# Performance work log

Hardware: AMD Instinct MI355X
Metric: run time of the kernel (lower is better)

The kernel has to match this reference:

```python
import jax, jax.numpy as jnp
import numpy as np

N = 32768       # total nodes across the batch of graphs
E = 524288      # total edges
D = 512         # feature dim (dimensions = [512, 512, 512])
G = 512         # number of graphs (64 nodes each)


def setup_inputs() -> dict:
    key = jax.random.key(0)
    ks = jax.random.split(key, 16)
    inp = {
        'feat': jax.random.normal(ks[0], (N, D), jnp.float32),
        'src': jax.random.randint(ks[1], (E,), 0, N, jnp.int32),
        'dst': jax.random.randint(ks[2], (E,), 0, N, jnp.int32),
        'adj_vals': jax.random.uniform(ks[3], (E,), jnp.float32),
        'graph_ids': (jnp.arange(N, dtype=jnp.int32) // (N // G)),
        'W0': jax.random.normal(ks[4], (D, D), jnp.float32) * 0.05,
        'b0': jnp.zeros((D,), jnp.float32),
        'W1': jax.random.normal(ks[5], (D, D), jnp.float32) * 0.05,
        'b1': jnp.zeros((D,), jnp.float32),
        'gW1': jax.random.normal(ks[6], (D, D), jnp.float32) * 0.05,
        'gb1': jnp.zeros((D,), jnp.float32),
        'gW2': jax.random.normal(ks[7], (D, D), jnp.float32) * 0.05,
        'gb2': jnp.zeros((D,), jnp.float32),
        'gW3': jax.random.normal(ks[8], (D, D), jnp.float32) * 0.05,
        'gb3': jnp.zeros((D,), jnp.float32),
        'gWs': jax.random.normal(ks[9], (D, D), jnp.float32) * 0.05,
        'gbs': jnp.zeros((D,), jnp.float32),
    }
    return inp


def reference(feat, src, dst, adj_vals, graph_ids,
              W0, b0, W1, b1,
              gW1, gb1, gW2, gb2, gW3, gb3, gWs, gbs):
    # GCN layer: act(A_hat @ (X W) + b), A_hat given as weighted edge list
    def gcn(h, W, b, act):
        support = h @ W                              # [N, D]
        msg = adj_vals[:, None] * support[src]       # [E, D]
        agg = jax.ops.segment_sum(msg, dst, num_segments=N)
        return act(agg + b)

    h = gcn(feat, W0, b0, jax.nn.relu)               # hidden layer, act=relu
    h = gcn(h, W1, b1, lambda x: x)                  # last layer, identity act

    # pooling: per-graph mean readout -> sigmoid -> repeat-expand back to nodes
    ones = jnp.ones((N, 1), h.dtype)
    counts = jax.ops.segment_sum(ones, graph_ids, num_segments=G)   # [G, 1]
    pooled = jax.ops.segment_sum(h, graph_ids, num_segments=G) / counts
    g = jax.nn.sigmoid(pooled)[graph_ids]            # [N, D] repeat-expanded

    z = jax.nn.relu(g @ gW1 + gb1)
    z = jax.nn.relu(z @ gW2 + gb2)
    z = jax.nn.relu(z @ gW3 + gb3)
    return z + (g @ gWs + gbs)
```

## Files before the change

kernel.cpp:

```cpp
#include <hip/hip_runtime.h>

typedef unsigned int u32;
typedef unsigned short u16;

typedef __attribute__((ext_vector_type(8))) __bf16 bf16x8;
typedef __attribute__((ext_vector_type(4))) float f32x4;
typedef __attribute__((ext_vector_type(2))) float f32x2;
typedef __attribute__((ext_vector_type(4))) u32 u32x4;

#define N_NODES 32768
#define N_EDGES 524288
#define DIM 512
#define N_GRAPHS 512
#define ECAP_ROW 1536
#define ECAP 1216
#define ELDS_SZ (ECAP + ECAP / 32 + 1)
#define NB_CONV 8192
#define NB_TR 1536

__device__ __forceinline__ u16 f2b(float f) {
  union { float f; u32 u; } v; v.f = f;
  u32 r = v.u + 0x7FFFu + ((v.u >> 16) & 1u);
  return (u16)(r >> 16);
}
__device__ __forceinline__ u32 pack2(float a, float b) {
  return (u32)f2b(a) | ((u32)f2b(b) << 16);
}
__device__ __forceinline__ float blo(u32 u) { union { u32 u; float f; } v; v.u = u << 16; return v.f; }
__device__ __forceinline__ float bhi(u32 u) { union { u32 u; float f; } v; v.u = u & 0xFFFF0000u; return v.f; }
__device__ __forceinline__ float b2f(u16 u) { union { u32 u; float f; } v; v.u = ((u32)u) << 16; return v.f; }

__device__ __forceinline__ void async16(const void* g, void* l) {
  __builtin_amdgcn_global_load_lds(
      (const __attribute__((address_space(1))) u32*)g,
      (__attribute__((address_space(3))) u32*)l, 16, 0, 0);
}

__device__ __forceinline__ int eidx(int i) { return i + (i >> 5); }

__device__ __forceinline__ void acc8(f32x2* a, u32x4 raw, float v) {
  f32x2 v2 = {v, v};
  a[0] += v2 * f32x2{blo(raw.x), bhi(raw.x)};
  a[1] += v2 * f32x2{blo(raw.y), bhi(raw.y)};
  a[2] += v2 * f32x2{blo(raw.z), bhi(raw.z)};
  a[3] += v2 * f32x2{blo(raw.w), bhi(raw.w)};
}

struct WPack {
  const float* src[6];
  u16* dst[6];
};
__global__ __launch_bounds__(256)
void k_prep(const float* __restrict__ feat, u16* __restrict__ featb, WPack wp,
            const int* __restrict__ dstv, int* __restrict__ counts) {
  __shared__ float tile[32][33];
  const int bid = blockIdx.x, tid = threadIdx.x;
  if (bid < NB_CONV) {
    int i = bid * 256 + tid;
    const float4* p = (const float4*)feat;
    float4 a = p[2 * i], b = p[2 * i + 1];
    uint4 o;
    o.x = pack2(a.x, a.y); o.y = pack2(a.z, a.w);
    o.z = pack2(b.x, b.y); o.w = pack2(b.z, b.w);
    ((uint4*)featb)[i] = o;
  } else if (bid < NB_CONV + NB_TR) {
    int idx = bid - NB_CONV;
    int bz = idx >> 8, rem = idx & 255, by = rem >> 4, bx = rem & 15;
    const float* W = wp.src[bz];
    u16* Wt = wp.dst[bz];
    int tx = tid & 31, ty = tid >> 5;
    int bx32 = bx * 32, by32 = by * 32;
    #pragma unroll
    for (int i = 0; i < 4; i++)
      tile[ty + 8 * i][tx] = W[(size_t)(by32 + ty + 8 * i) * DIM + bx32 + tx];
    __syncthreads();
    #pragma unroll
    for (int i = 0; i < 4; i++)
      Wt[(size_t)(bx32 + ty + 8 * i) * DIM + by32 + tx] = f2b(tile[tx][ty + 8 * i]);
  } else {
    int i = (bid - NB_CONV - NB_TR) * 256 + tid;
    atomicAdd(&counts[dstv[i]], 1);
  }
}

__global__ void k_scan(const int* __restrict__ counts, int* __restrict__ offsets,
                       int* __restrict__ cursor) {
  __shared__ int part[1024];
  int t = threadIdx.x;
  const int4* c4 = (const int4*)counts;
  int4 cv[8];
  #pragma unroll
  for (int j = 0; j < 8; j++) cv[j] = c4[t * 8 + j];
  int loc[32];
  int s = 0;
  #pragma unroll
  for (int j = 0; j < 8; j++) {
    loc[4 * j + 0] = s; s += cv[j].x;
    loc[4 * j + 1] = s; s += cv[j].y;
    loc[4 * j + 2] = s; s += cv[j].z;
    loc[4 * j + 3] = s; s += cv[j].w;
  }
  part[t] = s;
  __syncthreads();
  for (int off = 1; off < 1024; off <<= 1) {
    int v = (t >= off) ? part[t - off] : 0;
    __syncthreads();
    part[t] += v;
    __syncthreads();
  }
  int excl = (t == 0) ? 0 : part[t - 1];
  #pragma unroll
  for (int j = 0; j < 8; j++) {
    int4 o = make_int4(excl + loc[4 * j], excl + loc[4 * j + 1],
                       excl + loc[4 * j + 2], excl + loc[4 * j + 3]);
    ((int4*)offsets)[t * 8 + j] = o;
    ((int4*)cursor)[t * 8 + j] = o;
  }
  if (t == 1023) offsets[N_NODES] = excl + s;
}

__global__ void k_fill(const int* __restrict__ src, const int* __restrict__ dst,
                       const float* __restrict__ vals, int* __restrict__ cursor,
                       int2* __restrict__ epack) {
  int i = blockIdx.x * 256 + threadIdx.x;
  if (i >= N_EDGES) return;
  int d = dst[i];
  int p = atomicAdd(&cursor[d], 1);
  epack[p] = make_int2(src[i] | ((d & 63) << 15), __float_as_int(vals[i]));
}

__global__ __launch_bounds__(256)
void k_gemm_bt(const u16* __restrict__ A, const u16* __restrict__ Bt,
               u16* __restrict__ Cout, int M, int Nout, int K) {
  __shared__ __align__(16) u16 As[128 * 32];
  __shared__ __align__(16) u16 Bs[128 * 32];
  const int tid = threadIdx.x;
  const int l = tid & 63;
  const int w = tid >> 6;
  const int mBase = blockIdx.x * 128;
  const int nBase = blockIdx.y * 128;
  const int wm = (w >> 1) * 64;
  const int wn = (w & 1) * 64;
  const int lrow = l >> 2;
  const int lcol = (l & 3) * 8;
  const int q = l >> 4;
  const int r = l & 15;
  f32x4 acc[4][4] = {};

  for (int k0 = 0; k0 < K; k0 += 32) {
    #pragma unroll
    for (int p = 0; p < 2; p++) {
      int row = w * 32 + p * 16 + lrow;
      async16(A + (size_t)(mBase + row) * K + k0 + lcol, (char*)As + w * 2048 + p * 1024);
      async16(Bt + (size_t)(nBase + row) * K + k0 + lcol, (char*)Bs + w * 2048 + p * 1024);
    }
    __syncthreads();
    bf16x8 af[4], bfr[4];
    #pragma unroll
    for (int i = 0; i < 4; i++) af[i] = *(const bf16x8*)&As[(wm + i * 16 + r) * 32 + q * 8];
    #pragma unroll
    for (int j = 0; j < 4; j++) bfr[j] = *(const bf16x8*)&Bs[(wn + j * 16 + r) * 32 + q * 8];
    #pragma unroll
    for (int i = 0; i < 4; i++)
      #pragma unroll
      for (int j = 0; j < 4; j++)
        acc[i][j] = __builtin_amdgcn_mfma_f32_16x16x32_bf16(af[i], bfr[j], acc[i][j], 0, 0, 0);
    __syncthreads();
  }

  #pragma unroll
  for (int i = 0; i < 4; i++) {
    #pragma unroll
    for (int j = 0; j < 4; j++) {
      int col = nBase + wn + j * 16 + r;
      #pragma unroll
      for (int reg = 0; reg < 4; reg++) {
        int rowg = mBase + wm + i * 16 + q * 4 + reg;
        Cout[(size_t)rowg * Nout + col] = f2b(acc[i][j][reg]);
      }
    }
  }
}

template <bool RELU, bool ADDEND, bool OUTF32, bool SIGMOID>
__global__ __launch_bounds__(256)
void k_gemm_small(const u16* __restrict__ A, const u16* __restrict__ Bt,
                  const float* __restrict__ bias, const u16* __restrict__ addend,
                  void* __restrict__ Cout, int Nout, int K) {
  __shared__ __align__(16) u16 As[64 * 32];
  __shared__ __align__(16) u16 Bs[64 * 32];
  const int tid = threadIdx.x;
  const int l = tid & 63;
  const int w = tid >> 6;
  const int mBase = blockIdx.x * 64;
  const int nBase = blockIdx.y * 64;
  const int wm = (w >> 1) * 32;
  const int wn = (w & 1) * 32;
  const int lrow = tid >> 2;
  const int lcol = (tid & 3) * 8;
  const int q = l >> 4;
  const int r = l & 15;
  f32x4 acc[2][2] = {};

  for (int k0 = 0; k0 < K; k0 += 32) {
    async16(A + (size_t)(mBase + lrow) * K + k0 + lcol, (char*)As + tid * 16);
    async16(Bt + (size_t)(nBase + lrow) * K + k0 + lcol, (char*)Bs + tid * 16);
    __syncthreads();
    bf16x8 af[2], bfr[2];
    #pragma unroll
    for (int i = 0; i < 2; i++) af[i] = *(const bf16x8*)&As[(wm + i * 16 + r) * 32 + q * 8];
    #pragma unroll
    for (int j = 0; j < 2; j++) bfr[j] = *(const bf16x8*)&Bs[(wn + j * 16 + r) * 32 + q * 8];
    #pragma unroll
    for (int i = 0; i < 2; i++)
      #pragma unroll
      for (int j = 0; j < 2; j++)
        acc[i][j] = __builtin_amdgcn_mfma_f32_16x16x32_bf16(af[i], bfr[j], acc[i][j], 0, 0, 0);
    __syncthreads();
  }

  #pragma unroll
  for (int i = 0; i < 2; i++) {
    #pragma unroll
    for (int j = 0; j < 2; j++) {
      int col = nBase + wn + j * 16 + r;
      float bv = bias[col];
      #pragma unroll
      for (int reg = 0; reg < 4; reg++) {
        int rowg = mBase + wm + i * 16 + q * 4 + reg;
        float v = acc[i][j][reg] + bv;
        if (ADDEND) v += b2f(addend[(size_t)rowg * Nout + col]);
        if (RELU) v = fmaxf(v, 0.0f);
        if (SIGMOID) v = 1.0f / (1.0f + expf(-v));
        if (OUTF32) ((float*)Cout)[(size_t)rowg * Nout + col] = v;
        else ((u16*)Cout)[(size_t)rowg * Nout + col] = f2b(v);
      }
    }
  }
}

__global__ __launch_bounds__(256)
void k_agg_row(const u16* __restrict__ support, const int* __restrict__ offsets,
               const int2* __restrict__ epack, const float* __restrict__ bias,
               u16* __restrict__ outp) {
  __shared__ int2 eLds[ECAP_ROW];
  const int chunk = blockIdx.x & 7;
  const int cidx  = blockIdx.x >> 3;
  const int rowBase = cidx * 64;
  const int e0b = offsets[rowBase];
  const int nb = offsets[rowBase + 64] - e0b;
  for (int i = threadIdx.x; i < min(nb, ECAP_ROW); i += 256)
    eLds[i] = epack[e0b + i];
  __syncthreads();

  const int wi = threadIdx.x >> 6;
  const int l  = threadIdx.x & 63;
  const int grp = l >> 3;
  const int li  = l & 7;
  const int colOff = chunk * 64 + li * 8;
  const u16* spc = support + colOff;

  f32x2 b[4];
  {
    const float4* bp = (const float4*)(bias + colOff);
    float4 x = bp[0], y = bp[1];
    b[0] = f32x2{x.x, x.y}; b[1] = f32x2{x.z, x.w};
    b[2] = f32x2{y.x, y.y}; b[3] = f32x2{y.z, y.w};
  }

  #pragma unroll
  for (int pass = 0; pass < 2; pass++) {
    int r = rowBase + wi * 16 + pass * 8 + grp;
    int re0 = offsets[r] - e0b;
    int deg = offsets[r + 1] - e0b - re0;

    f32x2 a[4] = {b[0], b[1], b[2], b[3]};

    if (nb <= ECAP_ROW) {
      int i = 0;
      for (; i + 4 <= deg; i += 4) {
        int2 p0 = eLds[re0 + i];
        int2 p1 = eLds[re0 + i + 1];
        int2 p2 = eLds[re0 + i + 2];
        int2 p3 = eLds[re0 + i + 3];
        u32x4 r0 = *(const u32x4*)(spc + (size_t)(p0.x & 32767) * DIM);
        u32x4 r1 = *(const u32x4*)(spc + (size_t)(p1.x & 32767) * DIM);
        u32x4 r2 = *(const u32x4*)(spc + (size_t)(p2.x & 32767) * DIM);
        u32x4 r3 = *(const u32x4*)(spc + (size_t)(p3.x & 32767) * DIM);
        acc8(a, r0, __int_as_float(p0.y));
        acc8(a, r1, __int_as_float(p1.y));
        acc8(a, r2, __int_as_float(p2.y));
        acc8(a, r3, __int_as_float(p3.y));
      }
      for (; i < deg; i++) {
        int2 p = eLds[re0 + i];
        u32x4 raw = *(const u32x4*)(spc + (size_t)(p.x & 32767) * DIM);
        acc8(a, raw, __int_as_float(p.y));
      }
    } else {
      for (int i = 0; i < deg; i++) {
        int gi = re0 + i;
        int2 p = (gi < ECAP_ROW) ? eLds[gi] : epack[e0b + gi];
        u32x4 raw = *(const u32x4*)(spc + (size_t)(p.x & 32767) * DIM);
        acc8(a, raw, __int_as_float(p.y));
      }
    }

    #pragma unroll
    for (int i = 0; i < 4; i++) {
      a[i].x = fmaxf(a[i].x, 0.0f);
      a[i].y = fmaxf(a[i].y, 0.0f);
    }
    u32x4 o;
    o.x = pack2(a[0].x, a[0].y); o.y = pack2(a[1].x, a[1].y);
    o.z = pack2(a[2].x, a[2].y); o.w = pack2(a[3].x, a[3].y);
    *(u32x4*)(outp + (size_t)r * DIM + colOff) = o;
  }
}

__global__ __launch_bounds__(256)
void k_agg_pool(const u16* __restrict__ support, const int* __restrict__ offsets,
                const int2* __restrict__ epack, u16* __restrict__ outp) {
  __shared__ int2 eLds[ELDS_SZ];
  __shared__ float redLds[256];

  const int tid = threadIdx.x;
  const int chunk = blockIdx.x & 7;
  const int cidx = blockIdx.x >> 3;
  const int rowBase = cidx * 64;
  const int e0b = offsets[rowBase];
  const int nb = offsets[rowBase + 64] - e0b;
  const bool fits = (nb <= ECAP);

  if (fits) {
    for (int i = tid; i < nb; i += 256) eLds[eidx(i)] = epack[e0b + i];
  }
  __syncthreads();

  const int slot = tid >> 3;
  const int li = tid & 7;
  const int colOff = chunk * 64 + li * 8;
  const u16* spc = support + colOff;
  const int e0 = (nb * slot) >> 5;
  const int e1 = (nb * (slot + 1)) >> 5;

  f32x2 psum[4] = {};

  auto consume = [&](int2 p, u32x4 rw) {
    float v = __int_as_float(p.y);
    f32x2 v2 = {v, v};
    psum[0] += v2 * f32x2{blo(rw.x), bhi(rw.x)};
    psum[1] += v2 * f32x2{blo(rw.y), bhi(rw.y)};
    psum[2] += v2 * f32x2{blo(rw.z), bhi(rw.z)};
    psum[3] += v2 * f32x2{blo(rw.w), bhi(rw.w)};
  };

  if (fits) {
    int i = e0;
    for (; i + 8 <= e1; i += 8) {
      int2 p[8];
      #pragma unroll
      for (int j = 0; j < 8; j++) p[j] = eLds[eidx(i + j)];
      u32x4 rw[8];
      #pragma unroll
      for (int j = 0; j < 8; j++)
        rw[j] = *(const u32x4*)(spc + (size_t)(p[j].x & 32767) * DIM);
      #pragma unroll
      for (int j = 0; j < 8; j++) consume(p[j], rw[j]);
    }
    for (; i < e1; i++) {
      int2 p = eLds[eidx(i)];
      u32x4 rw = *(const u32x4*)(spc + (size_t)(p.x & 32767) * DIM);
      consume(p, rw);
    }
  } else {
    for (int i = e0; i < e1; i++) {
      int2 p = epack[e0b + i];
      u32x4 rw = *(const u32x4*)(spc + (size_t)(p.x & 32767) * DIM);
      consume(p, rw);
    }
  }

  #pragma unroll
  for (int k = 0; k < 4; k++) {
    psum[k].x += __shfl_xor(psum[k].x, 8);  psum[k].y += __shfl_xor(psum[k].y, 8);
    psum[k].x += __shfl_xor(psum[k].x, 16); psum[k].y += __shfl_xor(psum[k].y, 16);
    psum[k].x += __shfl_xor(psum[k].x, 32); psum[k].y += __shfl_xor(psum[k].y, 32);
  }
  const int wi = tid >> 6;
  if (((tid >> 3) & 7) == 0) {
    #pragma unroll
    for (int k = 0; k < 4; k++) {
      redLds[wi * 64 + li * 8 + 2 * k]     = psum[k].x;
      redLds[wi * 64 + li * 8 + 2 * k + 1] = psum[k].y;
    }
  }
  __syncthreads();
  if (tid < 64) {
    float s = redLds[tid] + redLds[64 + tid] + redLds[128 + tid] + redLds[192 + tid];
    outp[(size_t)cidx * DIM + chunk * 64 + tid] = f2b(s * (1.0f / 64.0f));
  }
}

__global__ void k_expand(const float* __restrict__ small, float* __restrict__ out) {
  int i = blockIdx.x * 256 + threadIdx.x;
  int col4 = i & 127;
  int node = i >> 7;
  float4 v = ((const float4*)small)[((node >> 6) << 7) + col4];
  ((float4*)out)[i] = v;
}

extern "C" void kernel_launch(void* const* d_in, const int* in_sizes, int n_in,
                              void* d_out, int out_size, void* d_ws, size_t ws_size,
                              hipStream_t stream) {
  const float* feat = (const float*)d_in[0];
  const int* src    = (const int*)d_in[1];
  const int* dst    = (const int*)d_in[2];
  const float* adj  = (const float*)d_in[3];
  const float* W0  = (const float*)d_in[5];
  const float* b0  = (const float*)d_in[6];
  const float* W1  = (const float*)d_in[7];
  const float* b1  = (const float*)d_in[8];
  const float* gW1 = (const float*)d_in[9];
  const float* gb1 = (const float*)d_in[10];
  const float* gW2 = (const float*)d_in[11];
  const float* gb2 = (const float*)d_in[12];
  const float* gW3 = (const float*)d_in[13];
  const float* gb3 = (const float*)d_in[14];
  const float* gWs = (const float*)d_in[15];
  const float* gbs = (const float*)d_in[16];

  char* ws = (char*)d_ws;
  size_t off = 0;
  auto alloc = [&](size_t bytes) -> void* {
    void* p = ws + off;
    off = (off + bytes + 255) & ~(size_t)255;
    return p;
  };
  u16* bufA = (u16*)alloc((size_t)N_NODES * DIM * 2);
  u16* bufB = (u16*)alloc((size_t)N_NODES * DIM * 2);
  u16* wt[6];
  for (int i = 0; i < 6; i++) wt[i] = (u16*)alloc((size_t)DIM * DIM * 2);
  int* counts   = (int*)alloc((size_t)N_NODES * 4);
  int* offsets  = (int*)alloc((size_t)(N_NODES + 1) * 4);
  int* cursor   = (int*)alloc((size_t)N_NODES * 4);
  int2* epack   = (int2*)alloc((size_t)N_EDGES * 8);
  u16* qb       = (u16*)alloc((size_t)N_GRAPHS * DIM * 2);
  u16* gfeat    = (u16*)alloc((size_t)N_GRAPHS * DIM * 2);
  u16* z1       = (u16*)alloc((size_t)N_GRAPHS * DIM * 2);
  u16* z2       = (u16*)alloc((size_t)N_GRAPHS * DIM * 2);
  u16* z3       = (u16*)alloc((size_t)N_GRAPHS * DIM * 2);
  float* osmall = (float*)alloc((size_t)N_GRAPHS * DIM * 4);

  (void)hipMemsetAsync(counts, 0, (size_t)N_NODES * 4, stream);

  WPack wp;
  wp.src[0] = W0; wp.src[1] = W1; wp.src[2] = gW1; wp.src[3] = gW2; wp.src[4] = gW3; wp.src[5] = gWs;
  for (int i = 0; i < 6; i++) wp.dst[i] = wt[i];

  k_prep<<<NB_CONV + NB_TR + N_EDGES / 256, 256, 0, stream>>>(feat, bufA, wp, dst, counts);
  k_scan<<<1, 1024, 0, stream>>>(counts, offsets, cursor);
  k_fill<<<N_EDGES / 256, 256, 0, stream>>>(src, dst, adj, cursor, epack);

  k_gemm_bt<<<dim3(N_NODES / 128, DIM / 128), 256, 0, stream>>>(bufA, wt[0], bufB, N_NODES, DIM, DIM);
  k_agg_row<<<4096, 256, 0, stream>>>(bufB, offsets, epack, b0, bufA);
  k_agg_pool<<<4096, 256, 0, stream>>>(bufA, offsets, epack, qb);
  k_gemm_small<false, false, false, true><<<dim3(8, 8), 256, 0, stream>>>(qb, wt[1], b1, nullptr, gfeat, DIM, DIM);

  k_gemm_small<true, false, false, false><<<dim3(8, 8), 256, 0, stream>>>(gfeat, wt[2], gb1, nullptr, z1, DIM, DIM);
  k_gemm_small<true, false, false, false><<<dim3(8, 8), 256, 0, stream>>>(z1, wt[3], gb2, nullptr, z2, DIM, DIM);
  k_gemm_small<true, false, false, false><<<dim3(8, 8), 256, 0, stream>>>(z2, wt[4], gb3, nullptr, z3, DIM, DIM);
  k_gemm_small<false, true, true, false><<<dim3(8, 8), 256, 0, stream>>>(gfeat, wt[5], gbs, z3, osmall, DIM, DIM);

  k_expand<<<(N_NODES * DIM / 4) / 256, 256, 0, stream>>>(osmall, (float*)d_out);
}
```

Measured before the change: 384.2 us.

## Edge-balance row aggregation with segmented LDS accumulation buckets

Each block's edges for its 64-row tile are now split evenly across 32 slots instead of giving each 8-lane group one destination row. Each slot accumulates per-row partial sums and writes them into one of three LDS buckets chosen by slot mod 3. A final pass sums the buckets, adds bias, applies ReLU and writes bf16. This targets imbalance from uneven node degrees. Staging of edge lists in LDS is dropped in both aggregation kernels in favour of direct global reads. Bucket writes overwrite rather than add, so a very high-degree row spanning slots that share a bucket would give wrong sums.

```diff
diff --git a/kernel.cpp b/kernel.cpp
--- a/kernel.cpp
+++ b/kernel.cpp
@@ -12,9 +12,6 @@
 #define N_EDGES 524288
 #define DIM 512
 #define N_GRAPHS 512
-#define ECAP_ROW 1536
-#define ECAP 1216
-#define ELDS_SZ (ECAP + ECAP / 32 + 1)
 #define NB_CONV 8192
 #define NB_TR 1536
 
@@ -35,8 +32,6 @@
       (const __attribute__((address_space(1))) u32*)g,
       (__attribute__((address_space(3))) u32*)l, 16, 0, 0);
 }
-
-__device__ __forceinline__ int eidx(int i) { return i + (i >> 5); }
 
 __device__ __forceinline__ void acc8(f32x2* a, u32x4 raw, float v) {
   f32x2 v2 = {v, v};
@@ -243,86 +238,7 @@
 void k_agg_row(const u16* __restrict__ support, const int* __restrict__ offsets,
                const int2* __restrict__ epack, const float* __restrict__ bias,
                u16* __restrict__ outp) {
-  __shared__ int2 eLds[ECAP_ROW];
-  const int chunk = blockIdx.x & 7;
-  const int cidx  = blockIdx.x >> 3;
-  const int rowBase = cidx * 64;
-  const int e0b = offsets[rowBase];
-  const int nb = offsets[rowBase + 64] - e0b;
-  for (int i = threadIdx.x; i < min(nb, ECAP_ROW); i += 256)
-    eLds[i] = epack[e0b + i];
-  __syncthreads();
-
-  const int wi = threadIdx.x >> 6;
-  const int l  = threadIdx.x & 63;
-  const int grp = l >> 3;
-  const int li  = l & 7;
-  const int colOff = chunk * 64 + li * 8;
-  const u16* spc = support + colOff;
-
-  f32x2 b[4];
-  {
-    const float4* bp = (const float4*)(bias + colOff);
-    float4 x = bp[0], y = bp[1];
-    b[0] = f32x2{x.x, x.y}; b[1] = f32x2{x.z, x.w};
-    b[2] = f32x2{y.x, y.y}; b[3] = f32x2{y.z, y.w};
-  }
-
-  #pragma unroll
-  for (int pass = 0; pass < 2; pass++) {
-    int r = rowBase + wi * 16 + pass * 8 + grp;
-    int re0 = offsets[r] - e0b;
-    int deg = offsets[r + 1] - e0b - re0;
-
-    f32x2 a[4] = {b[0], b[1], b[2], b[3]};
-
-    if (nb <= ECAP_ROW) {
-      int i = 0;
-      for (; i + 4 <= deg; i += 4) {
-        int2 p0 = eLds[re0 + i];
-        int2 p1 = eLds[re0 + i + 1];
-        int2 p2 = eLds[re0 + i + 2];
-        int2 p3 = eLds[re0 + i + 3];
-        u32x4 r0 = *(const u32x4*)(spc + (size_t)(p0.x & 32767) * DIM);
-        u32x4 r1 = *(const u32x4*)(spc + (size_t)(p1.x & 32767) * DIM);
-        u32x4 r2 = *(const u32x4*)(spc + (size_t)(p2.x & 32767) * DIM);
-        u32x4 r3 = *(const u32x4*)(spc + (size_t)(p3.x & 32767) * DIM);
-        acc8(a, r0, __int_as_float(p0.y));
-        acc8(a, r1, __int_as_float(p1.y));
-        acc8(a, r2, __int_as_float(p2.y));
-        acc8(a, r3, __int_as_float(p3.y));
-      }
-      for (; i < deg; i++) {
-        int2 p = eLds[re0 + i];
-        u32x4 raw = *(const u32x4*)(spc + (size_t)(p.x & 32767) * DIM);
-        acc8(a, raw, __int_as_float(p.y));
-      }
-    } else {
-      for (int i = 0; i < deg; i++) {
-        int gi = re0 + i;
-        int2 p = (gi < ECAP_ROW) ? eLds[gi] : epack[e0b + gi];
-        u32x4 raw = *(const u32x4*)(spc + (size_t)(p.x & 32767) * DIM);
-        acc8(a, raw, __int_as_float(p.y));
-      }
-    }
-
-    #pragma unroll
-    for (int i = 0; i < 4; i++) {
-      a[i].x = fmaxf(a[i].x, 0.0f);
-      a[i].y = fmaxf(a[i].y, 0.0f);
-    }
-    u32x4 o;
-    o.x = pack2(a[0].x, a[0].y); o.y = pack2(a[1].x, a[1].y);
-    o.z = pack2(a[2].x, a[2].y); o.w = pack2(a[3].x, a[3].y);
-    *(u32x4*)(outp + (size_t)r * DIM + colOff) = o;
-  }
-}
-
-__global__ __launch_bounds__(256)
-void k_agg_pool(const u16* __restrict__ support, const int* __restrict__ offsets,
-                const int2* __restrict__ epack, u16* __restrict__ outp) {
-  __shared__ int2 eLds[ELDS_SZ];
-  __shared__ float redLds[256];
+  __shared__ __align__(16) float accLds[3][64][66];
 
   const int tid = threadIdx.x;
   const int chunk = blockIdx.x & 7;
@@ -330,12 +246,97 @@
   const int rowBase = cidx * 64;
   const int e0b = offsets[rowBase];
   const int nb = offsets[rowBase + 64] - e0b;
-  const bool fits = (nb <= ECAP);
-
-  if (fits) {
-    for (int i = tid; i < nb; i += 256) eLds[eidx(i)] = epack[e0b + i];
+
+  {
+    f32x4 z = {};
+    f32x4* az = (f32x4*)&accLds[0][0][0];
+    for (int i = tid; i < 3168; i += 256) az[i] = z;
   }
   __syncthreads();
+
+  const int slot = tid >> 3;
+  const int li = tid & 7;
+  const int bucket = slot % 3;
+  const int colOff = chunk * 64 + li * 8;
+  const u16* spc = support + colOff;
+  const int e0 = (nb * slot) >> 5;
+  const int e1 = (nb * (slot + 1)) >> 5;
+
+  f32x2 a[4] = {};
+  int cur = -1;
+
+  auto flushRow = [&]() {
+    f32x2* ap = (f32x2*)&accLds[bucket][cur][li * 8];
+    ap[0] = a[0]; ap[1] = a[1]; ap[2] = a[2]; ap[3] = a[3];
+  };
+  auto step = [&](int2 p, u32x4 rw) {
+    int rr = p.x >> 15;
+    if (rr != cur) {
+      if (cur >= 0) flushRow();
+      cur = rr;
+      a[0] = f32x2{0.f, 0.f}; a[1] = f32x2{0.f, 0.f};
+      a[2] = f32x2{0.f, 0.f}; a[3] = f32x2{0.f, 0.f};
+    }
+    acc8(a, rw, __int_as_float(p.y));
+  };
+
+  int i = e0;
+  for (; i + 8 <= e1; i += 8) {
+    int2 p[8];
+    #pragma unroll
+    for (int j = 0; j < 8; j++) p[j] = epack[e0b + i + j];
+    u32x4 rw[8];
+    #pragma unroll
+    for (int j = 0; j < 8; j++)
+      rw[j] = *(const u32x4*)(spc + (size_t)(p[j].x & 32767) * DIM);
+    #pragma unroll
+    for (int j = 0; j < 8; j++) step(p[j], rw[j]);
+  }
+  for (; i < e1; i++) {
+    int2 p = epack[e0b + i];
+    u32x4 rw = *(const u32x4*)(spc + (size_t)(p.x & 32767) * DIM);
+    step(p, rw);
+  }
+  if (cur >= 0) flushRow();
+  __syncthreads();
+
+  const int r = tid >> 2;
+  const int cg = (tid & 3) * 16;
+  const int colBase = chunk * 64 + cg;
+  const float4* bp = (const float4*)(bias + colBase);
+  float vv[16];
+  #pragma unroll
+  for (int q4 = 0; q4 < 4; q4++) {
+    float4 b4 = bp[q4];
+    #pragma unroll
+    for (int t = 0; t < 4; t++) {
+      int c = cg + q4 * 4 + t;
+      float x = accLds[0][r][c] + accLds[1][r][c] + accLds[2][r][c]
+              + ((t == 0) ? b4.x : (t == 1) ? b4.y : (t == 2) ? b4.z : b4.w);
+      vv[q4 * 4 + t] = fmaxf(x, 0.0f);
+    }
+  }
+  u32x4 o0, o1;
+  o0.x = pack2(vv[0], vv[1]);   o0.y = pack2(vv[2], vv[3]);
+  o0.z = pack2(vv[4], vv[5]);   o0.w = pack2(vv[6], vv[7]);
+  o1.x = pack2(vv[8], vv[9]);   o1.y = pack2(vv[10], vv[11]);
+  o1.z = pack2(vv[12], vv[13]); o1.w = pack2(vv[14], vv[15]);
+  u16* op = outp + (size_t)(rowBase + r) * DIM + colBase;
+  *(u32x4*)op = o0;
+  *(u32x4*)(op + 8) = o1;
+}
+
+__global__ __launch_bounds__(256)
+void k_agg_pool(const u16* __restrict__ support, const int* __restrict__ offsets,
+                const int2* __restrict__ epack, u16* __restrict__ outp) {
+  __shared__ float redLds[256];
+
+  const int tid = threadIdx.x;
+  const int chunk = blockIdx.x & 7;
+  const int cidx = blockIdx.x >> 3;
+  const int rowBase = cidx * 64;
+  const int e0b = offsets[rowBase];
+  const int nb = offsets[rowBase + 64] - e0b;
 
   const int slot = tid >> 3;
   const int li = tid & 7;
@@ -355,30 +356,22 @@
     psum[3] += v2 * f32x2{blo(rw.w), bhi(rw.w)};
   };
 
-  if (fits) {
-    int i = e0;
-    for (; i + 8 <= e1; i += 8) {
-      int2 p[8];
-      #pragma unroll
-      for (int j = 0; j < 8; j++) p[j] = eLds[eidx(i + j)];
-      u32x4 rw[8];
-      #pragma unroll
-      for (int j = 0; j < 8; j++)
-        rw[j] = *(const u32x4*)(spc + (size_t)(p[j].x & 32767) * DIM);
-      #pragma unroll
-      for (int j = 0; j < 8; j++) consume(p[j], rw[j]);
-    }
-    for (; i < e1; i++) {
-      int2 p = eLds[eidx(i)];
-      u32x4 rw = *(const u32x4*)(spc + (size_t)(p.x & 32767) * DIM);
-      consume(p, rw);
-    }
-  } else {
-    for (int i = e0; i < e1; i++) {
-      int2 p = epack[e0b + i];
-      u32x4 rw = *(const u32x4*)(spc + (size_t)(p.x & 32767) * DIM);
-      consume(p, rw);
-    }
+  int i = e0;
+  for (; i + 8 <= e1; i += 8) {
+    int2 p[8];
+    #pragma unroll
+    for (int j = 0; j < 8; j++) p[j] = epack[e0b + i + j];
+    u32x4 rw[8];
+    #pragma unroll
+    for (int j = 0; j < 8; j++)
+      rw[j] = *(const u32x4*)(spc + (size_t)(p[j].x & 32767) * DIM);
+    #pragma unroll
+    for (int j = 0; j < 8; j++) consume(p[j], rw[j]);
+  }
+  for (; i < e1; i++) {
+    int2 p = epack[e0b + i];
+    u32x4 rw = *(const u32x4*)(spc + (size_t)(p.x & 32767) * DIM);
+    consume(p, rw);
   }
 
   #pragma unroll
```

Measured after the change: 415.1 us. 8.0% more time.

## Rebalance row aggregation with degree-sorted rows, smaller blocks and deeper unroll

Applied to the files above, without the earlier changes.

The first-layer row aggregation kernel now handles 32 rows per block instead of 64, doubling the grid so each 8-lane group processes one row rather than two. Rows inside the block are sorted by degree with a wave-level bitonic sort, so rows of similar degree share a wavefront and divergence drops. The gather loop is unrolled by 8 to keep more loads in flight. This costs an extra offsets read and sort per block, and the edge-staging buffer in shared memory is halved.

```diff
diff --git a/kernel.cpp b/kernel.cpp
--- a/kernel.cpp
+++ b/kernel.cpp
@@ -12,7 +12,7 @@
 #define N_EDGES 524288
 #define DIM 512
 #define N_GRAPHS 512
-#define ECAP_ROW 1536
+#define ECAP_ROW 768
 #define ECAP 1216
 #define ELDS_SZ (ECAP + ECAP / 32 + 1)
 #define NB_CONV 8192
@@ -244,78 +244,90 @@
                const int2* __restrict__ epack, const float* __restrict__ bias,
                u16* __restrict__ outp) {
   __shared__ int2 eLds[ECAP_ROW];
+  __shared__ unsigned char permLds[32];
+  const int tid = threadIdx.x;
   const int chunk = blockIdx.x & 7;
-  const int cidx  = blockIdx.x >> 3;
-  const int rowBase = cidx * 64;
+  const int gidx  = blockIdx.x >> 3;
+  const int rowBase = gidx * 32;
   const int e0b = offsets[rowBase];
-  const int nb = offsets[rowBase + 64] - e0b;
-  for (int i = threadIdx.x; i < min(nb, ECAP_ROW); i += 256)
-    eLds[i] = epack[e0b + i];
+  const int nb = offsets[rowBase + 32] - e0b;
+  const bool fits = (nb <= ECAP_ROW);
+
+  if (tid < 32) {
+    int deg = offsets[rowBase + tid + 1] - offsets[rowBase + tid];
+    u32 key = ((u32)deg << 8) | (u32)tid;
+    #pragma unroll
+    for (int k = 2; k <= 32; k <<= 1) {
+      #pragma unroll
+      for (int j = k >> 1; j >= 1; j >>= 1) {
+        u32 o = __shfl_xor(key, j);
+        bool lower = (tid & j) == 0;
+        bool asc = (tid & k) == 0;
+        key = ((key < o) == (lower == asc)) ? key : o;
+      }
+    }
+    permLds[tid] = (unsigned char)(key & 255u);
+  }
+  if (fits) {
+    for (int i = tid; i < nb; i += 256) eLds[i] = epack[e0b + i];
+  }
   __syncthreads();
 
-  const int wi = threadIdx.x >> 6;
-  const int l  = threadIdx.x & 63;
+  const int wi = tid >> 6;
+  const int l  = tid & 63;
   const int grp = l >> 3;
   const int li  = l & 7;
   const int colOff = chunk * 64 + li * 8;
   const u16* spc = support + colOff;
 
-  f32x2 b[4];
+  const int rl = permLds[wi * 8 + grp];
+  const int r = rowBase + rl;
+  const int re0 = offsets[r] - e0b;
+  const int deg = offsets[r + 1] - e0b - re0;
+
+  f32x2 a[4];
   {
     const float4* bp = (const float4*)(bias + colOff);
     float4 x = bp[0], y = bp[1];
-    b[0] = f32x2{x.x, x.y}; b[1] = f32x2{x.z, x.w};
-    b[2] = f32x2{y.x, y.y}; b[3] = f32x2{y.z, y.w};
-  }
-
-  #pragma unroll
-  for (int pass = 0; pass < 2; pass++) {
-    int r = rowBase + wi * 16 + pass * 8 + grp;
-    int re0 = offsets[r] - e0b;
-    int deg = offsets[r + 1] - e0b - re0;
-
-    f32x2 a[4] = {b[0], b[1], b[2], b[3]};
-
-    if (nb <= ECAP_ROW) {
-      int i = 0;
-      for (; i + 4 <= deg; i += 4) {
-        int2 p0 = eLds[re0 + i];
-        int2 p1 = eLds[re0 + i + 1];
-        int2 p2 = eLds[re0 + i + 2];
-        int2 p3 = eLds[re0 + i + 3];
-        u32x4 r0 = *(const u32x4*)(spc + (size_t)(p0.x & 32767) * DIM);
-        u32x4 r1 = *(const u32x4*)(spc + (size_t)(p1.x & 32767) * DIM);
-        u32x4 r2 = *(const u32x4*)(spc + (size_t)(p2.x & 32767) * DIM);
-        u32x4 r3 = *(const u32x4*)(spc + (size_t)(p3.x & 32767) * DIM);
-        acc8(a, r0, __int_as_float(p0.y));
-        acc8(a, r1, __int_as_float(p1.y));
-        acc8(a, r2, __int_as_float(p2.y));
-        acc8(a, r3, __int_as_float(p3.y));
-      }
-      for (; i < deg; i++) {
-        int2 p = eLds[re0 + i];
-        u32x4 raw = *(const u32x4*)(spc + (size_t)(p.x & 32767) * DIM);
-        acc8(a, raw, __int_as_float(p.y));
-      }
-    } else {
-      for (int i = 0; i < deg; i++) {
-        int gi = re0 + i;
-        int2 p = (gi < ECAP_ROW) ? eLds[gi] : epack[e0b + gi];
-        u32x4 raw = *(const u32x4*)(spc + (size_t)(p.x & 32767) * DIM);
-        acc8(a, raw, __int_as_float(p.y));
-      }
-    }
-
-    #pragma unroll
-    for (int i = 0; i < 4; i++) {
-      a[i].x = fmaxf(a[i].x, 0.0f);
-      a[i].y = fmaxf(a[i].y, 0.0f);
-    }
-    u32x4 o;
-    o.x = pack2(a[0].x, a[0].y); o.y = pack2(a[1].x, a[1].y);
-    o.z = pack2(a[2].x, a[2].y); o.w = pack2(a[3].x, a[3].y);
-    *(u32x4*)(outp + (size_t)r * DIM + colOff) = o;
-  }
+    a[0] = f32x2{x.x, x.y}; a[1] = f32x2{x.z, x.w};
+    a[2] = f32x2{y.x, y.y}; a[3] = f32x2{y.z, y.w};
+  }
+
+  if (fits) {
+    int i = 0;
+    for (; i + 8 <= deg; i += 8) {
+      int2 p[8];
+      #pragma unroll
+      for (int j = 0; j < 8; j++) p[j] = eLds[re0 + i + j];
+      u32x4 rw[8];
+      #pragma unroll
+      for (int j = 0; j < 8; j++)
+        rw[j] = *(const u32x4*)(spc + (size_t)(p[j].x & 32767) * DIM);
+      #pragma unroll
+      for (int j = 0; j < 8; j++) acc8(a, rw[j], __int_as_float(p[j].y));
+    }
+    for (; i < deg; i++) {
+      int2 p = eLds[re0 + i];
+      u32x4 rw = *(const u32x4*)(spc + (size_t)(p.x & 32767) * DIM);
+      acc8(a, rw, __int_as_float(p.y));
+    }
+  } else {
+    for (int i = 0; i < deg; i++) {
+      int2 p = epack[e0b + re0 + i];
+      u32x4 rw = *(const u32x4*)(spc + (size_t)(p.x & 32767) * DIM);
+      acc8(a, rw, __int_as_float(p.y));
+    }
+  }
+
+  #pragma unroll
+  for (int i = 0; i < 4; i++) {
+    a[i].x = fmaxf(a[i].x, 0.0f);
+    a[i].y = fmaxf(a[i].y, 0.0f);
+  }
+  u32x4 o;
+  o.x = pack2(a[0].x, a[0].y); o.y = pack2(a[1].x, a[1].y);
+  o.z = pack2(a[2].x, a[2].y); o.w = pack2(a[3].x, a[3].y);
+  *(u32x4*)(outp + (size_t)r * DIM + colOff) = o;
 }
 
 __global__ __launch_bounds__(256)
@@ -463,7 +475,7 @@
   k_fill<<<N_EDGES / 256, 256, 0, stream>>>(src, dst, adj, cursor, epack);
 
   k_gemm_bt<<<dim3(N_NODES / 128, DIM / 128), 256, 0, stream>>>(bufA, wt[0], bufB, N_NODES, DIM, DIM);
-  k_agg_row<<<4096, 256, 0, stream>>>(bufB, offsets, epack, b0, bufA);
+  k_agg_row<<<8192, 256, 0, stream>>>(bufB, offsets, epack, b0, bufA);
   k_agg_pool<<<4096, 256, 0, stream>>>(bufA, offsets, epack, qb);
   k_gemm_small<false, false, false, true><<<dim3(8, 8), 256, 0, stream>>>(qb, wt[1], b1, nullptr, gfeat, DIM, DIM);
 
```

New measurement: 383.9 us. Within noise of the previous version (-0.1%).
